# Optimization experiments

Hardware: AMD Instinct MI355X
Metric: run time of the kernel (lower is better)

Reference implementation:

```python
import jax, jax.numpy as jnp
import numpy as np

NEG_SLOPE = 0.2
EPS = 1e-16


def gat_conv(x, src, dst, W, a_src, a_dst, b, num_nodes):
    # Single-head PyG GATConv (heads=1, add_self_loops already applied via src/dst).
    h = x @ W                                   # [N, C]
    alpha_s = h @ a_src                         # [N]
    alpha_d = h @ a_dst                         # [N]
    e = jax.nn.leaky_relu(alpha_s[src] + alpha_d[dst], NEG_SLOPE)  # [E]
    # softmax over incoming edges per destination node
    m = jax.ops.segment_max(e, dst, num_segments=num_nodes)        # [N]
    ex = jnp.exp(e - m[dst])
    denom = jax.ops.segment_sum(ex, dst, num_segments=num_nodes)   # [N]
    alpha = ex / (denom[dst] + EPS)                                 # [E]
    out = jax.ops.segment_sum(h[src] * alpha[:, None], dst, num_segments=num_nodes)
    return out + b


def setup_inputs() -> dict:
    key = jax.random.key(0)
    ks = jax.random.split(key, 10)
    N, E, F_in, H, C = 100000, 1600000, 64, 64, 32
    x = jax.random.normal(ks[0], (N, F_in), dtype=jnp.float32)
    edge_index = jax.random.randint(ks[1], (2, E), 0, N, dtype=jnp.int64)
    s1 = 1.0 / np.sqrt(F_in)
    s2 = 1.0 / np.sqrt(H)
    return {
        "x": x,
        "edge_index": edge_index,
        "W1": jax.random.normal(ks[2], (F_in, H), dtype=jnp.float32) * s1,
        "a1_src": jax.random.normal(ks[3], (H,), dtype=jnp.float32) * s2,
        "a1_dst": jax.random.normal(ks[4], (H,), dtype=jnp.float32) * s2,
        "b1": jnp.zeros((H,), dtype=jnp.float32),
        "W2": jax.random.normal(ks[5], (H, C), dtype=jnp.float32) * s2,
        "a2_src": jax.random.normal(ks[6], (C,), dtype=jnp.float32) / np.sqrt(C),
        "a2_dst": jax.random.normal(ks[7], (C,), dtype=jnp.float32) / np.sqrt(C),
        "b2": jnp.zeros((C,), dtype=jnp.float32),
    }


def reference(x, edge_index, W1, a1_src, a1_dst, b1, W2, a2_src, a2_dst, b2):
    N = x.shape[0]
    loops = jnp.arange(N, dtype=edge_index.dtype)
    src = jnp.concatenate([edge_index[0], loops])  # add self-loops (GATConv default)
    dst = jnp.concatenate([edge_index[1], loops])
    # dropout layers are no-ops in eval mode
    h = jax.nn.relu(gat_conv(x, src, dst, W1, a1_src, a1_dst, b1, N))
    out = gat_conv(h, src, dst, W2, a2_src, a2_dst, b2, N)
    return jax.nn.log_softmax(out, axis=-1)
```

## Files before the change

### kernel.cpp

```cpp
#include <hip/hip_runtime.h>

typedef unsigned int uint;
typedef unsigned short ushort;
typedef short short8 __attribute__((ext_vector_type(8)));
typedef float floatx4 __attribute__((ext_vector_type(4)));

#define LEAKY(e) ((e) > 0.f ? (e) : 0.2f * (e))
#define BCAP 6144
#define EPT 32
#define TILE (256 * EPT)

__device__ __forceinline__ ushort f2bf(float f) {
    uint u = __float_as_uint(f);
    return (ushort)((u + 0x7fffu + ((u >> 16) & 1u)) >> 16);
}
__device__ __forceinline__ float bflo(uint u) { return __uint_as_float(u << 16); }
__device__ __forceinline__ float bfhi(uint u) { return __uint_as_float(u & 0xffff0000u); }

__global__ __launch_bounds__(256) void prepW(
    const float* __restrict__ W1, const float* __restrict__ W2,
    ushort* __restrict__ Wt1, ushort* __restrict__ Wt2)
{
    int t = blockIdx.x * 256 + threadIdx.x;
    if (t < 64 * 64) { int k = t >> 6, n = t & 63; Wt1[n * 64 + k] = f2bf(W1[t]); }
    if (t < 64 * 32) { int k = t >> 5, n = t & 31; Wt2[n * 64 + k] = f2bf(W2[t]); }
}

__global__ __launch_bounds__(256) void gemm1_mfma(
    const float* __restrict__ x, const ushort* __restrict__ Wt,
    const float* __restrict__ a_src, const float* __restrict__ a_dst,
    ushort* __restrict__ hb, float* __restrict__ as, float* __restrict__ ad, int N)
{
    int tid = threadIdx.x;
    int wave = tid >> 6, lane = tid & 63;
    int q = lane >> 4, c0 = lane & 15;
    int rowbase = blockIdx.x * 64 + wave * 16;
    int arow = rowbase + c0;
    bool aok = arow < N;

    short8 afrag[2];
#pragma unroll
    for (int kb = 0; kb < 2; ++kb) {
        float xa[8];
        if (aok) {
            const float4 u0 = *(const float4*)(x + (size_t)arow * 64 + kb * 32 + q * 8);
            const float4 u1 = *(const float4*)(x + (size_t)arow * 64 + kb * 32 + q * 8 + 4);
            xa[0] = u0.x; xa[1] = u0.y; xa[2] = u0.z; xa[3] = u0.w;
            xa[4] = u1.x; xa[5] = u1.y; xa[6] = u1.z; xa[7] = u1.w;
        } else {
#pragma unroll
            for (int j = 0; j < 8; ++j) xa[j] = 0.f;
        }
#pragma unroll
        for (int j = 0; j < 8; ++j) afrag[kb][j] = (short)f2bf(xa[j]);
    }

    short8 bfrag[4][2];
#pragma unroll
    for (int t = 0; t < 4; ++t)
#pragma unroll
        for (int kb = 0; kb < 2; ++kb)
            bfrag[t][kb] = *(const short8*)(Wt + (size_t)(t * 16 + c0) * 64 + kb * 32 + q * 8);

    floatx4 acc[4];
#pragma unroll
    for (int t = 0; t < 4; ++t) acc[t] = (floatx4){0.f, 0.f, 0.f, 0.f};
#pragma unroll
    for (int t = 0; t < 4; ++t)
#pragma unroll
        for (int kb = 0; kb < 2; ++kb)
            acc[t] = __builtin_amdgcn_mfma_f32_16x16x32_bf16(afrag[kb], bfrag[t][kb], acc[t], 0, 0, 0);

    float a_s[4], a_d[4];
#pragma unroll
    for (int t = 0; t < 4; ++t) { a_s[t] = a_src[t * 16 + c0]; a_d[t] = a_dst[t * 16 + c0]; }
    float vs[4], vd[4];
#pragma unroll
    for (int r = 0; r < 4; ++r) {
        vs[r] = 0.f; vd[r] = 0.f;
#pragma unroll
        for (int t = 0; t < 4; ++t) { vs[r] += acc[t][r] * a_s[t]; vd[r] += acc[t][r] * a_d[t]; }
    }
#pragma unroll
    for (int o = 1; o < 16; o <<= 1)
#pragma unroll
        for (int r = 0; r < 4; ++r) {
            vs[r] += __shfl_xor(vs[r], o, 16);
            vd[r] += __shfl_xor(vd[r], o, 16);
        }
    int drow = rowbase + q * 4;
    if (c0 == 0) {
#pragma unroll
        for (int r = 0; r < 4; ++r)
            if (drow + r < N) { as[drow + r] = vs[r]; ad[drow + r] = vd[r]; }
    }
#pragma unroll
    for (int r = 0; r < 4; ++r) {
        if (drow + r < N) {
#pragma unroll
            for (int t = 0; t < 4; ++t)
                hb[(size_t)(drow + r) * 64 + t * 16 + c0] = f2bf(acc[t][r]);
        }
    }
}

__global__ __launch_bounds__(256) void gemm2_mfma(
    const float* __restrict__ agg1, const float* __restrict__ b1,
    const ushort* __restrict__ Wt,
    const float* __restrict__ a_src, const float* __restrict__ a_dst,
    ushort* __restrict__ hb, float* __restrict__ as, float* __restrict__ ad, int N)
{
    int tid = threadIdx.x;
    int wave = tid >> 6, lane = tid & 63;
    int q = lane >> 4, c0 = lane & 15;
    int rowbase = blockIdx.x * 64 + wave * 16;
    int arow = rowbase + c0;
    bool aok = arow < N;

    short8 afrag[2];
#pragma unroll
    for (int kb = 0; kb < 2; ++kb) {
        float xa[8];
        const float4 b0 = *(const float4*)(b1 + kb * 32 + q * 8);
        const float4 b4 = *(const float4*)(b1 + kb * 32 + q * 8 + 4);
        if (aok) {
            const float4 u0 = *(const float4*)(agg1 + (size_t)arow * 64 + kb * 32 + q * 8);
            const float4 u1 = *(const float4*)(agg1 + (size_t)arow * 64 + kb * 32 + q * 8 + 4);
            xa[0] = u0.x + b0.x; xa[1] = u0.y + b0.y; xa[2] = u0.z + b0.z; xa[3] = u0.w + b0.w;
            xa[4] = u1.x + b4.x; xa[5] = u1.y + b4.y; xa[6] = u1.z + b4.z; xa[7] = u1.w + b4.w;
#pragma unroll
            for (int j = 0; j < 8; ++j) xa[j] = xa[j] > 0.f ? xa[j] : 0.f;
        } else {
#pragma unroll
            for (int j = 0; j < 8; ++j) xa[j] = 0.f;
        }
#pragma unroll
        for (int j = 0; j < 8; ++j) afrag[kb][j] = (short)f2bf(xa[j]);
    }

    short8 bfrag[2][2];
#pragma unroll
    for (int t = 0; t < 2; ++t)
#pragma unroll
        for (int kb = 0; kb < 2; ++kb)
            bfrag[t][kb] = *(const short8*)(Wt + (size_t)(t * 16 + c0) * 64 + kb * 32 + q * 8);

    floatx4 acc[2];
#pragma unroll
    for (int t = 0; t < 2; ++t) acc[t] = (floatx4){0.f, 0.f, 0.f, 0.f};
#pragma unroll
    for (int t = 0; t < 2; ++t)
#pragma unroll
        for (int kb = 0; kb < 2; ++kb)
            acc[t] = __builtin_amdgcn_mfma_f32_16x16x32_bf16(afrag[kb], bfrag[t][kb], acc[t], 0, 0, 0);

    float a_s[2], a_d[2];
#pragma unroll
    for (int t = 0; t < 2; ++t) { a_s[t] = a_src[t * 16 + c0]; a_d[t] = a_dst[t * 16 + c0]; }
    float vs[4], vd[4];
#pragma unroll
    for (int r = 0; r < 4; ++r) {
        vs[r] = 0.f; vd[r] = 0.f;
#pragma unroll
        for (int t = 0; t < 2; ++t) { vs[r] += acc[t][r] * a_s[t]; vd[r] += acc[t][r] * a_d[t]; }
    }
#pragma unroll
    for (int o = 1; o < 16; o <<= 1)
#pragma unroll
        for (int r = 0; r < 4; ++r) {
            vs[r] += __shfl_xor(vs[r], o, 16);
            vd[r] += __shfl_xor(vd[r], o, 16);
        }
    int drow = rowbase + q * 4;
    if (c0 == 0) {
#pragma unroll
        for (int r = 0; r < 4; ++r)
            if (drow + r < N) { as[drow + r] = vs[r]; ad[drow + r] = vd[r]; }
    }
#pragma unroll
    for (int r = 0; r < 4; ++r) {
        if (drow + r < N) {
#pragma unroll
            for (int t = 0; t < 2; ++t)
                hb[(size_t)(drow + r) * 32 + t * 16 + c0] = f2bf(acc[t][r]);
        }
    }
}

__global__ __launch_bounds__(256) void binK(
    const int* __restrict__ srcA, const int* __restrict__ dstA,
    int* __restrict__ bcur, int* __restrict__ binned, int E, int Etot, int nbuck)
{
    __shared__ int hist[512];
    __shared__ int basep[512];
    int t = threadIdx.x;
    long long start = (long long)blockIdx.x * TILE;

    hist[t] = 0; hist[t + 256] = 0;
    __syncthreads();

    short bs[EPT];
    int vals[EPT];
#pragma unroll
    for (int j = 0; j < EPT; ++j) {
        long long i = start + (long long)j * 256 + t;
        if (i < Etot) {
            int s, d;
            if (i < E) { s = srcA[i]; d = dstA[i]; } else { s = d = (int)(i - E); }
            int b = d >> 8;
            bs[j] = (short)b;
            vals[j] = (s << 8) | (d & 255);
            atomicAdd(&hist[b], 1);
        } else bs[j] = -1;
    }
    __syncthreads();

    for (int b = t; b < nbuck; b += 256) {
        int hc = hist[b];
        basep[b] = hc ? atomicAdd(bcur + b * 16, hc) : 0;
    }
    __syncthreads();
    hist[t] = 0; hist[t + 256] = 0;
    __syncthreads();

#pragma unroll
    for (int j = 0; j < EPT; ++j) {
        int b = bs[j];
        if (b >= 0) {
            int pos = basep[b] + atomicAdd(&hist[b], 1);
            if (pos < BCAP) binned[(size_t)b * BCAP + pos] = vals[j];
        }
    }
}

__global__ __launch_bounds__(512) void bscanK(
    const int* __restrict__ bcur, int* __restrict__ bbase,
    int* __restrict__ off, int nbuck, int N)
{
    __shared__ int sh[512];
    int t = threadIdx.x;
    int v = (t < nbuck) ? min(bcur[t * 16], BCAP) : 0;
    sh[t] = v;
    __syncthreads();
#pragma unroll
    for (int o = 1; o < 512; o <<= 1) {
        int u = (t >= o) ? sh[t - o] : 0;
        __syncthreads();
        sh[t] += u;
        __syncthreads();
    }
    if (t < nbuck) bbase[t] = sh[t] - v;
    if (t == 0) off[N] = sh[511];
}

__global__ __launch_bounds__(256) void bucketK(
    const int* __restrict__ bcur, const int* __restrict__ bbase,
    const int* __restrict__ binned, int* __restrict__ off,
    int* __restrict__ csr, int N)
{
    __shared__ int hist[256];
    __shared__ int sh[256];
    __shared__ int cur[256];
    int b = blockIdx.x;
    int t = threadIdx.x;
    int cnt = min(bcur[b * 16], BCAP);
    int base = bbase[b];
    const int* bin = binned + (size_t)b * BCAP;
    hist[t] = 0;
    __syncthreads();
    for (int i = t; i < cnt; i += 256) atomicAdd(&hist[bin[i] & 255], 1);
    __syncthreads();
    int v = hist[t];
    sh[t] = v;
    __syncthreads();
#pragma unroll
    for (int o = 1; o < 256; o <<= 1) {
        int u = (t >= o) ? sh[t - o] : 0;
        __syncthreads();
        sh[t] += u;
        __syncthreads();
    }
    int excl = sh[t] - v;
    int d = b * 256 + t;
    if (d < N) off[d] = base + excl;
    cur[t] = base + excl;
    __syncthreads();
    for (int i = t; i < cnt; i += 256) {
        int e = bin[i];
        int p = atomicAdd(&cur[e & 255], 1);
        csr[p] = e >> 8;
    }
}

__global__ __launch_bounds__(256) void node_agg1(
    const int* __restrict__ csr_src, const int* __restrict__ off,
    const float* __restrict__ as, const float* __restrict__ ad,
    const ushort* __restrict__ hb, float* __restrict__ agg, int N)
{
    int tid = threadIdx.x;
    int lid = tid & 7;
    int n = blockIdx.x * 32 + (tid >> 3);
    if (n >= N) return;
    int p0 = off[n], p1 = off[n + 1];
    float adn = ad[n];

    float den = 0.f;
    float acc[8];
#pragma unroll
    for (int k = 0; k < 8; ++k) acc[k] = 0.f;

    int p = p0;
    for (; p + 1 < p1; p += 2) {
        int s0 = csr_src[p], s1 = csr_src[p + 1];
        float w0 = __expf(LEAKY(as[s0] + adn));
        float w1 = __expf(LEAKY(as[s1] + adn));
        const uint4 v0 = *(const uint4*)(hb + (size_t)s0 * 64 + lid * 8);
        const uint4 v1 = *(const uint4*)(hb + (size_t)s1 * 64 + lid * 8);
        den += w0 + w1;
        acc[0] += w0 * bflo(v0.x); acc[1] += w0 * bfhi(v0.x);
        acc[2] += w0 * bflo(v0.y); acc[3] += w0 * bfhi(v0.y);
        acc[4] += w0 * bflo(v0.z); acc[5] += w0 * bfhi(v0.z);
        acc[6] += w0 * bflo(v0.w); acc[7] += w0 * bfhi(v0.w);
        acc[0] += w1 * bflo(v1.x); acc[1] += w1 * bfhi(v1.x);
        acc[2] += w1 * bflo(v1.y); acc[3] += w1 * bfhi(v1.y);
        acc[4] += w1 * bflo(v1.z); acc[5] += w1 * bfhi(v1.z);
        acc[6] += w1 * bflo(v1.w); acc[7] += w1 * bfhi(v1.w);
    }
    if (p < p1) {
        int s0 = csr_src[p];
        float w0 = __expf(LEAKY(as[s0] + adn));
        const uint4 v0 = *(const uint4*)(hb + (size_t)s0 * 64 + lid * 8);
        den += w0;
        acc[0] += w0 * bflo(v0.x); acc[1] += w0 * bfhi(v0.x);
        acc[2] += w0 * bflo(v0.y); acc[3] += w0 * bfhi(v0.y);
        acc[4] += w0 * bflo(v0.z); acc[5] += w0 * bfhi(v0.z);
        acc[6] += w0 * bflo(v0.w); acc[7] += w0 * bfhi(v0.w);
    }
    float inv = 1.f / den;
    float4 o0 = make_float4(acc[0] * inv, acc[1] * inv, acc[2] * inv, acc[3] * inv);
    float4 o1 = make_float4(acc[4] * inv, acc[5] * inv, acc[6] * inv, acc[7] * inv);
    float* op = agg + (size_t)n * 64 + lid * 8;
    *(float4*)op = o0;
    *(float4*)(op + 4) = o1;
}

__global__ __launch_bounds__(256) void node_agg2(
    const int* __restrict__ csr_src, const int* __restrict__ off,
    const float* __restrict__ as, const float* __restrict__ ad,
    const ushort* __restrict__ hb, const float* __restrict__ b2,
    float* __restrict__ out, int N)
{
    int tid = threadIdx.x;
    int lid = tid & 3;
    int n = blockIdx.x * 64 + (tid >> 2);
    if (n >= N) return;
    int p0 = off[n], p1 = off[n + 1];
    float adn = ad[n];

    float den = 0.f;
    float acc[8];
#pragma unroll
    for (int k = 0; k < 8; ++k) acc[k] = 0.f;

    int p = p0;
    for (; p + 1 < p1; p += 2) {
        int s0 = csr_src[p], s1 = csr_src[p + 1];
        float w0 = __expf(LEAKY(as[s0] + adn));
        float w1 = __expf(LEAKY(as[s1] + adn));
        const uint4 v0 = *(const uint4*)(hb + (size_t)s0 * 32 + lid * 8);
        const uint4 v1 = *(const uint4*)(hb + (size_t)s1 * 32 + lid * 8);
        den += w0 + w1;
        acc[0] += w0 * bflo(v0.x); acc[1] += w0 * bfhi(v0.x);
        acc[2] += w0 * bflo(v0.y); acc[3] += w0 * bfhi(v0.y);
        acc[4] += w0 * bflo(v0.z); acc[5] += w0 * bfhi(v0.z);
        acc[6] += w0 * bflo(v0.w); acc[7] += w0 * bfhi(v0.w);
        acc[0] += w1 * bflo(v1.x); acc[1] += w1 * bfhi(v1.x);
        acc[2] += w1 * bflo(v1.y); acc[3] += w1 * bfhi(v1.y);
        acc[4] += w1 * bflo(v1.z); acc[5] += w1 * bfhi(v1.z);
        acc[6] += w1 * bflo(v1.w); acc[7] += w1 * bfhi(v1.w);
    }
    if (p < p1) {
        int s0 = csr_src[p];
        float w0 = __expf(LEAKY(as[s0] + adn));
        const uint4 v0 = *(const uint4*)(hb + (size_t)s0 * 32 + lid * 8);
        den += w0;
        acc[0] += w0 * bflo(v0.x); acc[1] += w0 * bfhi(v0.x);
        acc[2] += w0 * bflo(v0.y); acc[3] += w0 * bfhi(v0.y);
        acc[4] += w0 * bflo(v0.z); acc[5] += w0 * bfhi(v0.z);
        acc[6] += w0 * bflo(v0.w); acc[7] += w0 * bfhi(v0.w);
    }
    float inv = 1.f / den;
#pragma unroll
    for (int k = 0; k < 8; ++k) acc[k] = acc[k] * inv + b2[lid * 8 + k];

    float mx = acc[0];
#pragma unroll
    for (int k = 1; k < 8; ++k) mx = fmaxf(mx, acc[k]);
#pragma unroll
    for (int o = 2; o > 0; o >>= 1) mx = fmaxf(mx, __shfl_xor(mx, o, 4));
    float se = 0.f;
#pragma unroll
    for (int k = 0; k < 8; ++k) se += __expf(acc[k] - mx);
#pragma unroll
    for (int o = 2; o > 0; o >>= 1) se += __shfl_xor(se, o, 4);
    float lse = mx + __logf(se);
    float4 o0 = make_float4(acc[0] - lse, acc[1] - lse, acc[2] - lse, acc[3] - lse);
    float4 o1 = make_float4(acc[4] - lse, acc[5] - lse, acc[6] - lse, acc[7] - lse);
    float* op = out + (size_t)n * 32 + lid * 8;
    *(float4*)op = o0;
    *(float4*)(op + 4) = o1;
}

extern "C" void kernel_launch(void* const* d_in, const int* in_sizes, int n_in,
                              void* d_out, int out_size, void* d_ws, size_t ws_size,
                              hipStream_t stream) {
    const float* x   = (const float*)d_in[0];
    const int*   ei  = (const int*)d_in[1];
    const float* W1  = (const float*)d_in[2];
    const float* a1s = (const float*)d_in[3];
    const float* a1d = (const float*)d_in[4];
    const float* b1  = (const float*)d_in[5];
    const float* W2  = (const float*)d_in[6];
    const float* a2s = (const float*)d_in[7];
    const float* a2d = (const float*)d_in[8];
    const float* b2  = (const float*)d_in[9];

    int N = in_sizes[0] / 64;
    int E = in_sizes[1] / 2;
    int Etot = E + N;
    int nbuck = (N + 255) >> 8;
    const int* srcA = ei;
    const int* dstA = ei + E;

    float* ws = (float*)d_ws;
    ushort* hb1 = (ushort*)ws;
    float* agg1 = ws + (size_t)N * 32;
    ushort* hb2 = (ushort*)(agg1 + (size_t)N * 64);
    float* as1  = agg1 + (size_t)N * 64 + (size_t)N * 16;
    float* ad1  = as1 + N;
    float* as2  = ad1 + N;
    float* ad2  = as2 + N;
    int* off    = (int*)(ad2 + N);
    int* bcur   = off + (N + 1);
    int* bbase  = bcur + (size_t)nbuck * 16;
    int* csr    = bbase + (nbuck + 1);
    int* binned = csr + Etot;
    ushort* Wt1 = (ushort*)(binned + (size_t)nbuck * BCAP);
    ushort* Wt2 = Wt1 + 64 * 64;

    hipMemsetAsync(bcur, 0, sizeof(int) * (size_t)nbuck * 16, stream);

    prepW<<<16, 256, 0, stream>>>(W1, W2, Wt1, Wt2);
    int tb = (int)(((long long)Etot + TILE - 1) / TILE);
    binK<<<tb, 256, 0, stream>>>(srcA, dstA, bcur, binned, E, Etot, nbuck);
    bscanK<<<1, 512, 0, stream>>>(bcur, bbase, off, nbuck, N);
    bucketK<<<nbuck, 256, 0, stream>>>(bcur, bbase, binned, off, csr, N);

    gemm1_mfma<<<(N + 63) / 64, 256, 0, stream>>>(x, Wt1, a1s, a1d, hb1, as1, ad1, N);
    node_agg1<<<(N + 31) / 32, 256, 0, stream>>>(csr, off, as1, ad1, hb1, agg1, N);

    gemm2_mfma<<<(N + 63) / 64, 256, 0, stream>>>(agg1, b1, Wt2, a2s, a2d, hb2, as2, ad2, N);
    node_agg2<<<(N + 63) / 64, 256, 0, stream>>>(csr, off, as2, ad2, hb2, b2,
                                                 (float*)d_out, N);
}
```

Before: 232.9 us.

## Drop prepW and bscanK launches, compute bucket base in-block, unroll edge loops by four

Removes the weight-transposition kernel by loading and converting the fp32 weights to bf16 directly inside both GEMM kernels. Removes the single-block bucket scan kernel: each bucket block now sums the counts of all earlier buckets with a block reduction, and the last block writes off[N]. The per-node aggregation loops are unrolled from two to four edges, with loads issued before the exps, to give more memory-level parallelism. This saves two launches and their serialization, at the cost of redundant prefix work (up to about 391 loads per block) and strided, uncoalesced weight loads in the GEMMs.

```diff
diff --git a/kernel.cpp b/kernel.cpp
--- a/kernel.cpp
+++ b/kernel.cpp
@@ -17,17 +17,8 @@
 __device__ __forceinline__ float bflo(uint u) { return __uint_as_float(u << 16); }
 __device__ __forceinline__ float bfhi(uint u) { return __uint_as_float(u & 0xffff0000u); }
 
-__global__ __launch_bounds__(256) void prepW(
-    const float* __restrict__ W1, const float* __restrict__ W2,
-    ushort* __restrict__ Wt1, ushort* __restrict__ Wt2)
-{
-    int t = blockIdx.x * 256 + threadIdx.x;
-    if (t < 64 * 64) { int k = t >> 6, n = t & 63; Wt1[n * 64 + k] = f2bf(W1[t]); }
-    if (t < 64 * 32) { int k = t >> 5, n = t & 31; Wt2[n * 64 + k] = f2bf(W2[t]); }
-}
-
 __global__ __launch_bounds__(256) void gemm1_mfma(
-    const float* __restrict__ x, const ushort* __restrict__ Wt,
+    const float* __restrict__ x, const float* __restrict__ W,
     const float* __restrict__ a_src, const float* __restrict__ a_dst,
     ushort* __restrict__ hb, float* __restrict__ as, float* __restrict__ ad, int N)
 {
@@ -60,7 +51,9 @@
     for (int t = 0; t < 4; ++t)
 #pragma unroll
         for (int kb = 0; kb < 2; ++kb)
-            bfrag[t][kb] = *(const short8*)(Wt + (size_t)(t * 16 + c0) * 64 + kb * 32 + q * 8);
+#pragma unroll
+            for (int j = 0; j < 8; ++j)
+                bfrag[t][kb][j] = (short)f2bf(W[(size_t)(kb * 32 + q * 8 + j) * 64 + t * 16 + c0]);
 
     floatx4 acc[4];
 #pragma unroll
@@ -106,7 +99,7 @@
 
 __global__ __launch_bounds__(256) void gemm2_mfma(
     const float* __restrict__ agg1, const float* __restrict__ b1,
-    const ushort* __restrict__ Wt,
+    const float* __restrict__ W,
     const float* __restrict__ a_src, const float* __restrict__ a_dst,
     ushort* __restrict__ hb, float* __restrict__ as, float* __restrict__ ad, int N)
 {
@@ -143,7 +136,9 @@
     for (int t = 0; t < 2; ++t)
 #pragma unroll
         for (int kb = 0; kb < 2; ++kb)
-            bfrag[t][kb] = *(const short8*)(Wt + (size_t)(t * 16 + c0) * 64 + kb * 32 + q * 8);
+#pragma unroll
+            for (int j = 0; j < 8; ++j)
+                bfrag[t][kb][j] = (short)f2bf(W[(size_t)(kb * 32 + q * 8 + j) * 32 + t * 16 + c0]);
 
     floatx4 acc[2];
 #pragma unroll
@@ -233,30 +228,9 @@
     }
 }
 
-__global__ __launch_bounds__(512) void bscanK(
-    const int* __restrict__ bcur, int* __restrict__ bbase,
-    int* __restrict__ off, int nbuck, int N)
-{
-    __shared__ int sh[512];
-    int t = threadIdx.x;
-    int v = (t < nbuck) ? min(bcur[t * 16], BCAP) : 0;
-    sh[t] = v;
-    __syncthreads();
-#pragma unroll
-    for (int o = 1; o < 512; o <<= 1) {
-        int u = (t >= o) ? sh[t - o] : 0;
-        __syncthreads();
-        sh[t] += u;
-        __syncthreads();
-    }
-    if (t < nbuck) bbase[t] = sh[t] - v;
-    if (t == 0) off[N] = sh[511];
-}
-
 __global__ __launch_bounds__(256) void bucketK(
-    const int* __restrict__ bcur, const int* __restrict__ bbase,
-    const int* __restrict__ binned, int* __restrict__ off,
-    int* __restrict__ csr, int N)
+    const int* __restrict__ bcur, const int* __restrict__ binned,
+    int* __restrict__ off, int* __restrict__ csr, int N, int nbuck)
 {
     __shared__ int hist[256];
     __shared__ int sh[256];
@@ -264,8 +238,20 @@
     int b = blockIdx.x;
     int t = threadIdx.x;
     int cnt = min(bcur[b * 16], BCAP);
-    int base = bbase[b];
     const int* bin = binned + (size_t)b * BCAP;
+
+    int partial = 0;
+    for (int i = t; i < b; i += 256) partial += min(bcur[i * 16], BCAP);
+    sh[t] = partial;
+    __syncthreads();
+#pragma unroll
+    for (int o = 128; o > 0; o >>= 1) {
+        if (t < o) sh[t] += sh[t + o];
+        __syncthreads();
+    }
+    int base = sh[0];
+    __syncthreads();
+
     hist[t] = 0;
     __syncthreads();
     for (int i = t; i < cnt; i += 256) atomicAdd(&hist[bin[i] & 255], 1);
@@ -283,6 +269,7 @@
     int excl = sh[t] - v;
     int d = b * 256 + t;
     if (d < N) off[d] = base + excl;
+    if (b == nbuck - 1 && t == 0) off[N] = base + cnt;
     cur[t] = base + excl;
     __syncthreads();
     for (int i = t; i < cnt; i += 256) {
@@ -310,13 +297,18 @@
     for (int k = 0; k < 8; ++k) acc[k] = 0.f;
 
     int p = p0;
-    for (; p + 1 < p1; p += 2) {
-        int s0 = csr_src[p], s1 = csr_src[p + 1];
-        float w0 = __expf(LEAKY(as[s0] + adn));
-        float w1 = __expf(LEAKY(as[s1] + adn));
+    for (; p + 3 < p1; p += 4) {
+        int s0 = csr_src[p], s1 = csr_src[p + 1], s2 = csr_src[p + 2], s3 = csr_src[p + 3];
+        float e0 = as[s0], e1 = as[s1], e2 = as[s2], e3 = as[s3];
         const uint4 v0 = *(const uint4*)(hb + (size_t)s0 * 64 + lid * 8);
         const uint4 v1 = *(const uint4*)(hb + (size_t)s1 * 64 + lid * 8);
-        den += w0 + w1;
+        const uint4 v2 = *(const uint4*)(hb + (size_t)s2 * 64 + lid * 8);
+        const uint4 v3 = *(const uint4*)(hb + (size_t)s3 * 64 + lid * 8);
+        float w0 = __expf(LEAKY(e0 + adn));
+        float w1 = __expf(LEAKY(e1 + adn));
+        float w2 = __expf(LEAKY(e2 + adn));
+        float w3 = __expf(LEAKY(e3 + adn));
+        den += (w0 + w1) + (w2 + w3);
         acc[0] += w0 * bflo(v0.x); acc[1] += w0 * bfhi(v0.x);
         acc[2] += w0 * bflo(v0.y); acc[3] += w0 * bfhi(v0.y);
         acc[4] += w0 * bflo(v0.z); acc[5] += w0 * bfhi(v0.z);
@@ -325,8 +317,16 @@
         acc[2] += w1 * bflo(v1.y); acc[3] += w1 * bfhi(v1.y);
         acc[4] += w1 * bflo(v1.z); acc[5] += w1 * bfhi(v1.z);
         acc[6] += w1 * bflo(v1.w); acc[7] += w1 * bfhi(v1.w);
-    }
-    if (p < p1) {
+        acc[0] += w2 * bflo(v2.x); acc[1] += w2 * bfhi(v2.x);
+        acc[2] += w2 * bflo(v2.y); acc[3] += w2 * bfhi(v2.y);
+        acc[4] += w2 * bflo(v2.z); acc[5] += w2 * bfhi(v2.z);
+        acc[6] += w2 * bflo(v2.w); acc[7] += w2 * bfhi(v2.w);
+        acc[0] += w3 * bflo(v3.x); acc[1] += w3 * bfhi(v3.x);
+        acc[2] += w3 * bflo(v3.y); acc[3] += w3 * bfhi(v3.y);
+        acc[4] += w3 * bflo(v3.z); acc[5] += w3 * bfhi(v3.z);
+        acc[6] += w3 * bflo(v3.w); acc[7] += w3 * bfhi(v3.w);
+    }
+    for (; p < p1; ++p) {
         int s0 = csr_src[p];
         float w0 = __expf(LEAKY(as[s0] + adn));
         const uint4 v0 = *(const uint4*)(hb + (size_t)s0 * 64 + lid * 8);
@@ -363,13 +363,18 @@
     for (int k = 0; k < 8; ++k) acc[k] = 0.f;
 
     int p = p0;
-    for (; p + 1 < p1; p += 2) {
-        int s0 = csr_src[p], s1 = csr_src[p + 1];
-        float w0 = __expf(LEAKY(as[s0] + adn));
-        float w1 = __expf(LEAKY(as[s1] + adn));
+    for (; p + 3 < p1; p += 4) {
+        int s0 = csr_src[p], s1 = csr_src[p + 1], s2 = csr_src[p + 2], s3 = csr_src[p + 3];
+        float e0 = as[s0], e1 = as[s1], e2 = as[s2], e3 = as[s3];
         const uint4 v0 = *(const uint4*)(hb + (size_t)s0 * 32 + lid * 8);
         const uint4 v1 = *(const uint4*)(hb + (size_t)s1 * 32 + lid * 8);
-        den += w0 + w1;
+        const uint4 v2 = *(const uint4*)(hb + (size_t)s2 * 32 + lid * 8);
+        const uint4 v3 = *(const uint4*)(hb + (size_t)s3 * 32 + lid * 8);
+        float w0 = __expf(LEAKY(e0 + adn));
+        float w1 = __expf(LEAKY(e1 + adn));
+        float w2 = __expf(LEAKY(e2 + adn));
+        float w3 = __expf(LEAKY(e3 + adn));
+        den += (w0 + w1) + (w2 + w3);
         acc[0] += w0 * bflo(v0.x); acc[1] += w0 * bfhi(v0.x);
         acc[2] += w0 * bflo(v0.y); acc[3] += w0 * bfhi(v0.y);
         acc[4] += w0 * bflo(v0.z); acc[5] += w0 * bfhi(v0.z);
@@ -378,8 +383,16 @@
         acc[2] += w1 * bflo(v1.y); acc[3] += w1 * bfhi(v1.y);
         acc[4] += w1 * bflo(v1.z); acc[5] += w1 * bfhi(v1.z);
         acc[6] += w1 * bflo(v1.w); acc[7] += w1 * bfhi(v1.w);
-    }
-    if (p < p1) {
+        acc[0] += w2 * bflo(v2.x); acc[1] += w2 * bfhi(v2.x);
+        acc[2] += w2 * bflo(v2.y); acc[3] += w2 * bfhi(v2.y);
+        acc[4] += w2 * bflo(v2.z); acc[5] += w2 * bfhi(v2.z);
+        acc[6] += w2 * bflo(v2.w); acc[7] += w2 * bfhi(v2.w);
+        acc[0] += w3 * bflo(v3.x); acc[1] += w3 * bfhi(v3.x);
+        acc[2] += w3 * bflo(v3.y); acc[3] += w3 * bfhi(v3.y);
+        acc[4] += w3 * bflo(v3.z); acc[5] += w3 * bfhi(v3.z);
+        acc[6] += w3 * bflo(v3.w); acc[7] += w3 * bfhi(v3.w);
+    }
+    for (; p < p1; ++p) {
         int s0 = csr_src[p];
         float w0 = __expf(LEAKY(as[s0] + adn));
         const uint4 v0 = *(const uint4*)(hb + (size_t)s0 * 32 + lid * 8);
@@ -442,24 +455,19 @@
     float* ad2  = as2 + N;
     int* off    = (int*)(ad2 + N);
     int* bcur   = off + (N + 1);
-    int* bbase  = bcur + (size_t)nbuck * 16;
-    int* csr    = bbase + (nbuck + 1);
+    int* csr    = bcur + (size_t)nbuck * 16;
     int* binned = csr + Etot;
-    ushort* Wt1 = (ushort*)(binned + (size_t)nbuck * BCAP);
-    ushort* Wt2 = Wt1 + 64 * 64;
 
     hipMemsetAsync(bcur, 0, sizeof(int) * (size_t)nbuck * 16, stream);
 
-    prepW<<<16, 256, 0, stream>>>(W1, W2, Wt1, Wt2);
     int tb = (int)(((long long)Etot + TILE - 1) / TILE);
     binK<<<tb, 256, 0, stream>>>(srcA, dstA, bcur, binned, E, Etot, nbuck);
-    bscanK<<<1, 512, 0, stream>>>(bcur, bbase, off, nbuck, N);
-    bucketK<<<nbuck, 256, 0, stream>>>(bcur, bbase, binned, off, csr, N);
-
-    gemm1_mfma<<<(N + 63) / 64, 256, 0, stream>>>(x, Wt1, a1s, a1d, hb1, as1, ad1, N);
+    bucketK<<<nbuck, 256, 0, stream>>>(bcur, binned, off, csr, N, nbuck);
+
+    gemm1_mfma<<<(N + 63) / 64, 256, 0, stream>>>(x, W1, a1s, a1d, hb1, as1, ad1, N);
     node_agg1<<<(N + 31) / 32, 256, 0, stream>>>(csr, off, as1, ad1, hb1, agg1, N);
 
-    gemm2_mfma<<<(N + 63) / 64, 256, 0, stream>>>(agg1, b1, Wt2, a2s, a2d, hb2, as2, ad2, N);
+    gemm2_mfma<<<(N + 63) / 64, 256, 0, stream>>>(agg1, b1, W2, a2s, a2d, hb2, as2, ad2, N);
     node_agg2<<<(N + 63) / 64, 256, 0, stream>>>(csr, off, as2, ad2, hb2, b2,
                                                  (float*)d_out, N);
 }
```

Measured after the change: 225.1 us. 1.03x faster.
